# Optimization experiments

Hardware: AMD Instinct MI355X
Metric: run time of the kernel (lower is better)

Reference implementation:

```python
import math
import jax, jax.numpy as jnp
import numpy as np

N, T, D, H = 256, 128, 1024, 1024


def setup_inputs() -> dict:
    key = jax.random.key(0)
    k1, k2, k3, k4, k5 = jax.random.split(key, 5)
    x = jax.random.normal(k1, (N, T, D), dtype=jnp.float32)
    A = jax.random.normal(k2, (N, H, 4, 4), dtype=jnp.float32)
    Wx = jax.random.normal(k3, (D, 4 * H), dtype=jnp.float32) / math.sqrt(D)
    Wh = jax.random.normal(k4, (H, 4 * H), dtype=jnp.float32) / math.sqrt(H)
    Wattn = jax.random.normal(k5, (H, 4 * H), dtype=jnp.float32) / math.sqrt(H)
    b = jnp.zeros((4 * H,), dtype=jnp.float32)
    return {"x": x, "A": A, "Wx": Wx, "Wh": Wh, "Wattn": Wattn, "b": b}


def reference(x, A, Wx, Wh, Wattn, b):
    n, h = A.shape[0], A.shape[1]
    Af = A.reshape(n, h, 16)           # (N, H, 16) flattened 4x4 feature map
    h0 = Af.mean(axis=2)               # mean-pooled global feature inits h0, c0
    scale = 1.0 / math.sqrt(h)

    def step(carry, x_t):
        prev_h, prev_c = carry
        # scaled dot-product attention over 16 spatial locations
        logits = jnp.einsum("nh,nhl->nl", prev_h, Af) * scale   # (N, 16)
        w = jax.nn.softmax(logits, axis=1)
        attn = jnp.einsum("nhl,nl->nh", Af, w)                  # (N, H)
        # LSTM gates
        pre = x_t @ Wx + prev_h @ Wh + attn @ Wattn + b          # (N, 4H)
        i, f, o, g = jnp.split(pre, 4, axis=1)
        next_c = jax.nn.sigmoid(f) * prev_c + jax.nn.sigmoid(i) * jnp.tanh(g)
        next_h = jax.nn.sigmoid(o) * jnp.tanh(next_c)
        return (next_h, next_c), next_h

    xs = jnp.swapaxes(x, 0, 1)         # (T, N, D)
    _, hs = jax.lax.scan(step, (h0, h0), xs)
    return jnp.swapaxes(hs, 0, 1)      # (N, T, H)
```

## Files before the change

kernel.cpp:

```cpp
#include <hip/hip_runtime.h>
#include <hip/hip_bf16.h>

#define NB 256
#define TT 128
#define DD 1024
#define HH 1024
#define FH 4096
#define KTOT 3072

typedef __attribute__((ext_vector_type(4))) float f32x4;
typedef __attribute__((ext_vector_type(8))) short short8;
typedef __attribute__((ext_vector_type(4))) unsigned u32x4;

__device__ __forceinline__ unsigned short f2bf(float f) {
    union { float f; unsigned u; } v; v.f = f;
    unsigned u = v.u;
    u += 0x7FFFu + ((u >> 16) & 1u);
    return (unsigned short)(u >> 16);
}
__device__ __forceinline__ float bf2f(unsigned short u) {
    union { unsigned u; float f; } v; v.u = ((unsigned)u) << 16; return v.f;
}
__device__ __forceinline__ float sigm(float v) { return 1.f / (1.f + __expf(-v)); }
__device__ __forceinline__ float tanhf_(float v) { return 1.f - 2.f / (__expf(2.f * v) + 1.f); }

__device__ __forceinline__ void bmap(int bid, int& m0, int& j0) {
    int xx = bid & 7, yy = (bid >> 3) & 7, mt = bid >> 6;
    m0 = mt * 64;
    j0 = (xx * 8 + yy) * 16;
}

__device__ __forceinline__ short8 pack8(float4 v0, float4 v1) {
    short8 r;
    r[0] = (short)f2bf(v0.x); r[1] = (short)f2bf(v0.y);
    r[2] = (short)f2bf(v0.z); r[3] = (short)f2bf(v0.w);
    r[4] = (short)f2bf(v1.x); r[5] = (short)f2bf(v1.y);
    r[6] = (short)f2bf(v1.z); r[7] = (short)f2bf(v1.w);
    return r;
}

__global__ __launch_bounds__(256) void wt_prep(const float* __restrict__ Wx,
                                               const float* __restrict__ Wh,
                                               const float* __restrict__ Wattn,
                                               unsigned short* __restrict__ Wt) {
    __shared__ unsigned short tile[64][65];
    int k0 = blockIdx.x * 64;
    int c0 = blockIdx.y * 64;
    const float* src; int kl0;
    if (k0 < 1024)      { src = Wx;    kl0 = k0; }
    else if (k0 < 2048) { src = Wh;    kl0 = k0 - 1024; }
    else                { src = Wattn; kl0 = k0 - 2048; }
    int tid = threadIdx.x;
    int r = tid >> 2;
    int ch = (tid & 3) << 4;
    const float* p = src + (size_t)(kl0 + r) * FH + c0 + ch;
#pragma unroll
    for (int i = 0; i < 16; i += 4) {
        float4 v = *reinterpret_cast<const float4*>(p + i);
        tile[r][ch + i + 0] = f2bf(v.x);
        tile[r][ch + i + 1] = f2bf(v.y);
        tile[r][ch + i + 2] = f2bf(v.z);
        tile[r][ch + i + 3] = f2bf(v.w);
    }
    __syncthreads();
    alignas(16) unsigned short vals[16];
#pragma unroll
    for (int i = 0; i < 16; ++i) vals[i] = tile[ch + i][r];
    unsigned short* q = Wt + (size_t)(c0 + r) * KTOT + k0 + ch;
    *reinterpret_cast<uint4*>(q)     = *reinterpret_cast<uint4*>(&vals[0]);
    *reinterpret_cast<uint4*>(q + 8) = *reinterpret_cast<uint4*>(&vals[8]);
}

__global__ __launch_bounds__(256) void zero_buf(float* __restrict__ p, int n) {
    int i = blockIdx.x * 256 + threadIdx.x;
    if (i < n) p[i] = 0.f;
}

__global__ __launch_bounds__(256) void xconv(const float* __restrict__ x,
                                             unsigned short* __restrict__ xbf) {
    size_t i = ((size_t)blockIdx.x * 256 + threadIdx.x) * 8;
    float4 v0 = *reinterpret_cast<const float4*>(x + i);
    float4 v1 = *reinterpret_cast<const float4*>(x + i + 4);
    short8 p = pack8(v0, v1);
    *reinterpret_cast<short8*>(xbf + i) = p;
}

__global__ __launch_bounds__(256) void afT_prep(const float* __restrict__ A,
                                                unsigned short* __restrict__ AfT) {
    int n = blockIdx.x;
#pragma unroll
    for (int pass = 0; pass < 4; ++pass) {
        int hh = pass * 256 + threadIdx.x;
        const float4* p = reinterpret_cast<const float4*>(A + ((size_t)n * HH + hh) * 16);
        float4 a0 = p[0], a1 = p[1], a2 = p[2], a3 = p[3];
        float av[16] = {a0.x,a0.y,a0.z,a0.w, a1.x,a1.y,a1.z,a1.w,
                        a2.x,a2.y,a2.z,a2.w, a3.x,a3.y,a3.z,a3.w};
#pragma unroll
        for (int l = 0; l < 16; ++l)
            AfT[((size_t)n * 16 + l) * HH + hh] = f2bf(av[l]);
    }
}

__global__ __launch_bounds__(256) void g_gemm(const unsigned short* __restrict__ AfT,
                                              const unsigned short* __restrict__ Wt,
                                              unsigned short* __restrict__ G) {
    int mt = blockIdx.y;
    int ct = blockIdx.x;
    int tid = threadIdx.x;
    int w = tid >> 6, lane = tid & 63;
    int wm = w >> 1, wn = w & 1;
    int cw = lane & 15, k8 = (lane >> 4) << 3;

    const unsigned short* ap[4];
    const unsigned short* bp[4];
#pragma unroll
    for (int mf = 0; mf < 4; ++mf)
        ap[mf] = AfT + (size_t)(mt * 128 + wm * 64 + mf * 16 + cw) * HH + k8;
#pragma unroll
    for (int fn = 0; fn < 4; ++fn)
        bp[fn] = Wt + (size_t)(ct * 128 + wn * 64 + fn * 16 + cw) * KTOT + 2048 + k8;

    f32x4 acc[4][4];
#pragma unroll
    for (int mf = 0; mf < 4; ++mf)
#pragma unroll
        for (int fn = 0; fn < 4; ++fn)
#pragma unroll
            for (int e = 0; e < 4; ++e) acc[mf][fn][e] = 0.f;

#pragma unroll 4
    for (int ch = 0; ch < 32; ++ch) {
        short8 a[4], b[4];
#pragma unroll
        for (int i = 0; i < 4; ++i)
            a[i] = *reinterpret_cast<const short8*>(ap[i] + ch * 32);
#pragma unroll
        for (int i = 0; i < 4; ++i)
            b[i] = *reinterpret_cast<const short8*>(bp[i] + ch * 32);
#pragma unroll
        for (int mf = 0; mf < 4; ++mf)
#pragma unroll
            for (int fn = 0; fn < 4; ++fn)
                acc[mf][fn] = __builtin_amdgcn_mfma_f32_16x16x32_bf16(
                    a[mf], b[fn], acc[mf][fn], 0, 0, 0);
    }

    int l0 = (lane >> 4) << 2;
#pragma unroll
    for (int mf = 0; mf < 4; ++mf) {
        int n = mt * 8 + wm * 4 + mf;
#pragma unroll
        for (int fn = 0; fn < 4; ++fn) {
            int cc = ct * 128 + wn * 64 + fn * 16 + cw;
            unsigned lo = (unsigned)f2bf(acc[mf][fn][0]) | ((unsigned)f2bf(acc[mf][fn][1]) << 16);
            unsigned hi = (unsigned)f2bf(acc[mf][fn][2]) | ((unsigned)f2bf(acc[mf][fn][3]) << 16);
            uint2 val; val.x = lo; val.y = hi;
            *reinterpret_cast<uint2*>(G + ((size_t)n * FH + cc) * 16 + l0) = val;
        }
    }
}

template<bool PF32>
__global__ __launch_bounds__(256)
void xw_gemm(const float* __restrict__ x, const unsigned short* __restrict__ Wt,
             const float* __restrict__ bb, void* __restrict__ prex) {
    int ct = blockIdx.x;
    int mt = blockIdx.y;
    int tid = threadIdx.x;
    int w = tid >> 6, lane = tid & 63;
    int wm = w >> 1, wn = w & 1;
    int cw = lane & 15, k8 = (lane >> 4) << 3;

    const float* ap[4];
    const unsigned short* bp[4];
#pragma unroll
    for (int mf = 0; mf < 4; ++mf)
        ap[mf] = x + (size_t)(mt * 128 + wm * 64 + mf * 16 + cw) * DD + k8;
#pragma unroll
    for (int fn = 0; fn < 4; ++fn)
        bp[fn] = Wt + (size_t)(ct * 128 + wn * 64 + fn * 16 + cw) * KTOT + k8;

    f32x4 acc[4][4];
#pragma unroll
    for (int mf = 0; mf < 4; ++mf)
#pragma unroll
        for (int fn = 0; fn < 4; ++fn)
#pragma unroll
            for (int e = 0; e < 4; ++e) acc[mf][fn][e] = 0.f;

#pragma unroll 2
    for (int ch = 0; ch < 32; ++ch) {
        short8 a[4]; short8 b[4];
#pragma unroll
        for (int i = 0; i < 4; ++i) {
            float4 u0 = *reinterpret_cast<const float4*>(ap[i] + ch * 32);
            float4 u1 = *reinterpret_cast<const float4*>(ap[i] + ch * 32 + 4);
            a[i] = pack8(u0, u1);
        }
#pragma unroll
        for (int i = 0; i < 4; ++i)
            b[i] = *reinterpret_cast<const short8*>(bp[i] + ch * 32);
#pragma unroll
        for (int mf = 0; mf < 4; ++mf)
#pragma unroll
            for (int fn = 0; fn < 4; ++fn)
                acc[mf][fn] = __builtin_amdgcn_mfma_f32_16x16x32_bf16(
                    a[mf], b[fn], acc[mf][fn], 0, 0, 0);
    }

    int r0 = (lane >> 4) << 2;
#pragma unroll
    for (int fn = 0; fn < 4; ++fn) {
        int cc = ct * 128 + wn * 64 + fn * 16 + cw;
        float bv = bb[cc];
#pragma unroll
        for (int mf = 0; mf < 4; ++mf) {
            size_t row = (size_t)(mt * 128 + wm * 64 + mf * 16 + r0);
#pragma unroll
            for (int e = 0; e < 4; ++e) {
                float v = acc[mf][fn][e] + bv;
                if (PF32) ((float*)prex)[(row + e) * FH + cc] = v;
                else      ((unsigned short*)prex)[(row + e) * FH + cc] = f2bf(v);
            }
        }
    }
}

__global__ __launch_bounds__(512) void init_kernel(const float* __restrict__ A,
                                                   float* __restrict__ c,
                                                   unsigned short* __restrict__ h0,
                                                   float* __restrict__ lg0) {
    int m0, j0; bmap(blockIdx.x, m0, j0);
    int tid = threadIdx.x;
    int r = tid >> 3, j2 = (tid & 7) * 2;
    int n = m0 + r;
    float lg[16];
#pragma unroll
    for (int l = 0; l < 16; ++l) lg[l] = 0.f;
#pragma unroll
    for (int e = 0; e < 2; ++e) {
        int j = j0 + j2 + e;
        const float4* p = reinterpret_cast<const float4*>(A + ((size_t)n * HH + j) * 16);
        float4 a0 = p[0], a1 = p[1], a2 = p[2], a3 = p[3];
        float av[16] = {a0.x,a0.y,a0.z,a0.w, a1.x,a1.y,a1.z,a1.w,
                        a2.x,a2.y,a2.z,a2.w, a3.x,a3.y,a3.z,a3.w};
        float s = 0.f;
#pragma unroll
        for (int l = 0; l < 16; ++l) s += av[l];
        float m = s * 0.0625f;
        c[(size_t)n * HH + j] = m;
        h0[(size_t)n * HH + j] = f2bf(m);
#pragma unroll
        for (int l = 0; l < 16; ++l) lg[l] += m * av[l];
    }
#pragma unroll
    for (int l = 0; l < 16; ++l) {
        lg[l] += __shfl_xor(lg[l], 1);
        lg[l] += __shfl_xor(lg[l], 2);
        lg[l] += __shfl_xor(lg[l], 4);
    }
    int l0 = (tid & 7) * 2;
    atomicAdd(&lg0[(size_t)n * 16 + l0],     lg[l0]);
    atomicAdd(&lg0[(size_t)n * 16 + l0 + 1], lg[l0 + 1]);
}

template<bool PF32>
__global__ __launch_bounds__(256, 4)
void step_prex(const void* __restrict__ prex,
               const unsigned short* __restrict__ hprev, unsigned short* __restrict__ hnext,
               const unsigned short* __restrict__ Wt, const unsigned short* __restrict__ G,
               const unsigned short* __restrict__ AfT,
               const float* __restrict__ lgcur, float* __restrict__ lgnext,
               float* __restrict__ lgz, float* __restrict__ c,
               float* __restrict__ out, int t) {
    __shared__ float red[2][64][20];
    __shared__ float hn_s[16][16];

    const int bid = blockIdx.x;
    const int jt = (bid & 7) * 8 + ((bid >> 3) & 7);
    const int mt = bid >> 6;
    const int m0 = mt * 16, j0 = jt * 16;
    const int tid = threadIdx.x;
    const int wk = tid >> 6, lane = tid & 63;
    const int cw = lane & 15, k8 = (lane >> 4) << 3;

    const unsigned short* bp[4];
#pragma unroll
    for (int fn = 0; fn < 4; ++fn)
        bp[fn] = Wt + (size_t)(fn * 1024 + j0 + cw) * KTOT + 1024 + wk * 256 + k8;
    const unsigned short* ap = hprev + (size_t)(m0 + cw) * HH + wk * 256 + k8;

    f32x4 acc[4];
#pragma unroll
    for (int fn = 0; fn < 4; ++fn)
#pragma unroll
        for (int e = 0; e < 4; ++e) acc[fn][e] = 0.f;

#pragma unroll
    for (int ch = 0; ch < 8; ++ch) {
        short8 a = *reinterpret_cast<const short8*>(ap + ch * 32);
        short8 b[4];
#pragma unroll
        for (int i = 0; i < 4; ++i)
            b[i] = *reinterpret_cast<const short8*>(bp[i] + ch * 32);
#pragma unroll
        for (int fn = 0; fn < 4; ++fn)
            acc[fn] = __builtin_amdgcn_mfma_f32_16x16x32_bf16(a, b[fn], acc[fn], 0, 0, 0);
    }

    const int r0 = (lane >> 4) << 2;
    if (wk < 2) {
#pragma unroll
        for (int fn = 0; fn < 4; ++fn)
            *reinterpret_cast<f32x4*>(&red[wk][fn * 16 + cw][r0]) = acc[fn];
    }
    __syncthreads();
    if (wk >= 2) {
#pragma unroll
        for (int fn = 0; fn < 4; ++fn) {
            float* p = &red[wk - 2][fn * 16 + cw][r0];
            f32x4 v = *reinterpret_cast<const f32x4*>(p);
            v += acc[fn];
            *reinterpret_cast<f32x4*>(p) = v;
        }
    }
    __syncthreads();

    const int er = tid >> 4, ej = tid & 15;
    const int en = m0 + er, ejj = j0 + ej;

    const u32x4* gb = reinterpret_cast<const u32x4*>(G + ((size_t)en * FH + ejj) * 16);
    u32x4 gv[8];
#pragma unroll
    for (int g = 0; g < 4; ++g) {
        gv[g * 2]     = gb[g * 2048];
        gv[g * 2 + 1] = gb[g * 2048 + 1];
    }
    float pxv[4];
    {
        size_t prow = ((size_t)en * TT + t) * FH + ejj;
#pragma unroll
        for (int g = 0; g < 4; ++g) {
            if (PF32) pxv[g] = ((const float*)prex)[prow + g * 1024];
            else      pxv[g] = bf2f(((const unsigned short*)prex)[prow + g * 1024]);
        }
    }
    float cv = c[(size_t)en * HH + ejj];

    float sm[16];
    {
        const float4* lp = reinterpret_cast<const float4*>(lgcur + (size_t)en * 16);
        float4 s0 = lp[0], s1 = lp[1], s2 = lp[2], s3 = lp[3];
        float sv[16] = {s0.x,s0.y,s0.z,s0.w, s1.x,s1.y,s1.z,s1.w,
                        s2.x,s2.y,s2.z,s2.w, s3.x,s3.y,s3.z,s3.w};
        float mx = -1e30f;
#pragma unroll
        for (int l = 0; l < 16; ++l) { sv[l] *= 0.03125f; mx = fmaxf(mx, sv[l]); }
        float sum = 0.f;
#pragma unroll
        for (int l = 0; l < 16; ++l) { sm[l] = __expf(sv[l] - mx); sum += sm[l]; }
        float inv = 1.f / sum;
#pragma unroll
        for (int l = 0; l < 16; ++l) sm[l] *= inv;
    }

    float pre[4];
#pragma unroll
    for (int g = 0; g < 4; ++g) {
        float p = red[0][g * 16 + ej][er] + red[1][g * 16 + ej][er] + pxv[g];
        float d = 0.f;
#pragma unroll
        for (int q = 0; q < 4; ++q) {
            d += sm[q * 2]     * bf2f((unsigned short)(gv[g * 2][q] & 0xFFFF));
            d += sm[q * 2 + 1] * bf2f((unsigned short)(gv[g * 2][q] >> 16));
        }
#pragma unroll
        for (int q = 0; q < 4; ++q) {
            d += sm[8 + q * 2]     * bf2f((unsigned short)(gv[g * 2 + 1][q] & 0xFFFF));
            d += sm[8 + q * 2 + 1] * bf2f((unsigned short)(gv[g * 2 + 1][q] >> 16));
        }
        pre[g] = p + d;
    }

    float ig = sigm(pre[0]);
    float fg = sigm(pre[1]);
    float og = sigm(pre[2]);
    float gg = tanhf_(pre[3]);
    float cn = fg * cv + ig * gg;
    float hn = og * tanhf_(cn);
    c[(size_t)en * HH + ejj] = cn;
    hnext[(size_t)en * HH + ejj] = f2bf(hn);
    __builtin_nontemporal_store(hn, out + ((size_t)en * TT + t) * HH + ejj);
    hn_s[er][ej] = hn;
    if (jt == 0) lgz[(size_t)en * 16 + ej] = 0.f;
    __syncthreads();

    const unsigned short* afp = AfT + ((size_t)en * 16 + ej) * HH + j0;
    uint4 q0 = *reinterpret_cast<const uint4*>(afp);
    uint4 q1 = *reinterpret_cast<const uint4*>(afp + 8);
    const unsigned* au = reinterpret_cast<const unsigned*>(&q0);
    const unsigned* av = reinterpret_cast<const unsigned*>(&q1);
    float part = 0.f;
#pragma unroll
    for (int q = 0; q < 4; ++q) {
        part += hn_s[er][q * 2]     * bf2f((unsigned short)(au[q] & 0xFFFF));
        part += hn_s[er][q * 2 + 1] * bf2f((unsigned short)(au[q] >> 16));
    }
#pragma unroll
    for (int q = 0; q < 4; ++q) {
        part += hn_s[er][8 + q * 2]     * bf2f((unsigned short)(av[q] & 0xFFFF));
        part += hn_s[er][8 + q * 2 + 1] * bf2f((unsigned short)(av[q] >> 16));
    }
    atomicAdd(&lgnext[(size_t)en * 16 + ej], part);
}

template<bool XBF>
__global__ __launch_bounds__(256, 4)
void gemm_step(const float* __restrict__ x, const unsigned short* __restrict__ xbf,
               const unsigned short* __restrict__ hprev, unsigned short* __restrict__ hnext,
               const unsigned short* __restrict__ Wt, const unsigned short* __restrict__ G,
               const unsigned short* __restrict__ AfT, const float* __restrict__ bb,
               const float* __restrict__ lgcur, float* __restrict__ lgnext,
               float* __restrict__ lgz, float* __restrict__ c,
               float* __restrict__ out, int t) {
    __shared__ float red[2][64][36];
    __shared__ float hn_s[32][16];

    const int bid = blockIdx.x;
    const int jt = (bid & 7) * 8 + ((bid >> 3) & 7);
    const int mt = bid >> 6;
    const int m0 = mt * 32, j0 = jt * 16;
    const int tid = threadIdx.x;
    const int wk = tid >> 6, lane = tid & 63;
    const int cw = lane & 15, k8 = (lane >> 4) << 3;

    const unsigned short* bp[4];
#pragma unroll
    for (int fn = 0; fn < 4; ++fn)
        bp[fn] = Wt + (size_t)(fn * 1024 + j0 + cw) * KTOT + wk * 512 + k8;

    f32x4 acc[2][4];
#pragma unroll
    for (int mf = 0; mf < 2; ++mf)
#pragma unroll
        for (int fn = 0; fn < 4; ++fn)
#pragma unroll
            for (int e = 0; e < 4; ++e) acc[mf][fn][e] = 0.f;

    if (wk < 2) {
        if (XBF) {
            const unsigned short* ap[2];
#pragma unroll
            for (int mf = 0; mf < 2; ++mf)
                ap[mf] = xbf + ((size_t)(m0 + mf * 16 + cw) * TT + t) * DD + wk * 512 + k8;
#pragma unroll 4
            for (int ch = 0; ch < 16; ++ch) {
                short8 a[2], b[4];
#pragma unroll
                for (int i = 0; i < 2; ++i)
                    a[i] = *reinterpret_cast<const short8*>(ap[i] + ch * 32);
#pragma unroll
                for (int i = 0; i < 4; ++i)
                    b[i] = *reinterpret_cast<const short8*>(bp[i] + ch * 32);
#pragma unroll
                for (int mf = 0; mf < 2; ++mf)
#pragma unroll
                    for (int fn = 0; fn < 4; ++fn)
                        acc[mf][fn] = __builtin_amdgcn_mfma_f32_16x16x32_bf16(
                            a[mf], b[fn], acc[mf][fn], 0, 0, 0);
            }
        } else {
            const float* ap[2];
#pragma unroll
            for (int mf = 0; mf < 2; ++mf)
                ap[mf] = x + ((size_t)(m0 + mf * 16 + cw) * TT + t) * DD + wk * 512 + k8;
#pragma unroll 2
            for (int ch = 0; ch < 16; ++ch) {
                short8 a[2], b[4];
#pragma unroll
                for (int i = 0; i < 2; ++i) {
                    float4 u0 = *reinterpret_cast<const float4*>(ap[i] + ch * 32);
                    float4 u1 = *reinterpret_cast<const float4*>(ap[i] + ch * 32 + 4);
                    a[i] = pack8(u0, u1);
                }
#pragma unroll
                for (int i = 0; i < 4; ++i)
                    b[i] = *reinterpret_cast<const short8*>(bp[i] + ch * 32);
#pragma unroll
                for (int mf = 0; mf < 2; ++mf)
#pragma unroll
                    for (int fn = 0; fn < 4; ++fn)
                        acc[mf][fn] = __builtin_amdgcn_mfma_f32_16x16x32_bf16(
                            a[mf], b[fn], acc[mf][fn], 0, 0, 0);
            }
        }
    } else {
        const unsigned short* ap[2];
#pragma unroll
        for (int mf = 0; mf < 2; ++mf)
            ap[mf] = hprev + (size_t)(m0 + mf * 16 + cw) * HH + (wk - 2) * 512 + k8;
#pragma unroll 4
        for (int ch = 0; ch < 16; ++ch) {
            short8 a[2], b[4];
#pragma unroll
            for (int i = 0; i < 2; ++i)
                a[i] = *reinterpret_cast<const short8*>(ap[i] + ch * 32);
#pragma unroll
            for (int i = 0; i < 4; ++i)
                b[i] = *reinterpret_cast<const short8*>(bp[i] + ch * 32);
#pragma unroll
            for (int mf = 0; mf < 2; ++mf)
#pragma unroll
                for (int fn = 0; fn < 4; ++fn)
                    acc[mf][fn] = __builtin_amdgcn_mfma_f32_16x16x32_bf16(
                        a[mf], b[fn], acc[mf][fn], 0, 0, 0);
        }
    }

    const int r0 = (lane >> 4) << 2;
    if (wk < 2) {
#pragma unroll
        for (int mf = 0; mf < 2; ++mf)
#pragma unroll
            for (int fn = 0; fn < 4; ++fn)
                *reinterpret_cast<f32x4*>(&red[wk][fn * 16 + cw][mf * 16 + r0]) = acc[mf][fn];
    }
    __syncthreads();
    if (wk >= 2) {
#pragma unroll
        for (int mf = 0; mf < 2; ++mf)
#pragma unroll
            for (int fn = 0; fn < 4; ++fn) {
                float* p = &red[wk - 2][fn * 16 + cw][mf * 16 + r0];
                f32x4 v = *reinterpret_cast<const f32x4*>(p);
                v += acc[mf][fn];
                *reinterpret_cast<f32x4*>(p) = v;
            }
    }
    __syncthreads();

    const bool zeroer = (jt == 0);
#pragma unroll
    for (int s = 0; s < 2; ++s) {
        int task = tid + s * 256;
        int er = task >> 4, ej = task & 15;
        int en = m0 + er, ejj = j0 + ej;

        const u32x4* gb = reinterpret_cast<const u32x4*>(G + ((size_t)en * FH + ejj) * 16);
        u32x4 gv[8];
#pragma unroll
        for (int g = 0; g < 4; ++g) {
            gv[g * 2]     = gb[g * 2048];
            gv[g * 2 + 1] = gb[g * 2048 + 1];
        }
        float cv = c[(size_t)en * HH + ejj];

        float sm[16];
        {
            const float4* lp = reinterpret_cast<const float4*>(lgcur + (size_t)en * 16);
            float4 s0 = lp[0], s1 = lp[1], s2 = lp[2], s3 = lp[3];
            float sv[16] = {s0.x,s0.y,s0.z,s0.w, s1.x,s1.y,s1.z,s1.w,
                            s2.x,s2.y,s2.z,s2.w, s3.x,s3.y,s3.z,s3.w};
            float mx = -1e30f;
#pragma unroll
            for (int l = 0; l < 16; ++l) { sv[l] *= 0.03125f; mx = fmaxf(mx, sv[l]); }
            float sum = 0.f;
#pragma unroll
            for (int l = 0; l < 16; ++l) { sm[l] = __expf(sv[l] - mx); sum += sm[l]; }
            float inv = 1.f / sum;
#pragma unroll
            for (int l = 0; l < 16; ++l) sm[l] *= inv;
        }

        float pre[4];
#pragma unroll
        for (int g = 0; g < 4; ++g) {
            float p = red[0][g * 16 + ej][er] + red[1][g * 16 + ej][er] + bb[g * HH + ejj];
            float d = 0.f;
#pragma unroll
            for (int q = 0; q < 4; ++q) {
                d += sm[q * 2]     * bf2f((unsigned short)(gv[g * 2][q] & 0xFFFF));
                d += sm[q * 2 + 1] * bf2f((unsigned short)(gv[g * 2][q] >> 16));
            }
#pragma unroll
            for (int q = 0; q < 4; ++q) {
                d += sm[8 + q * 2]     * bf2f((unsigned short)(gv[g * 2 + 1][q] & 0xFFFF));
                d += sm[8 + q * 2 + 1] * bf2f((unsigned short)(gv[g * 2 + 1][q] >> 16));
            }
            pre[g] = p + d;
        }

        float ig = sigm(pre[0]);
        float fg = sigm(pre[1]);
        float og = sigm(pre[2]);
        float gg = tanhf_(pre[3]);
        float cn = fg * cv + ig * gg;
        float hn = og * tanhf_(cn);
        c[(size_t)en * HH + ejj] = cn;
        hnext[(size_t)en * HH + ejj] = f2bf(hn);
        __builtin_nontemporal_store(hn, out + ((size_t)en * TT + t) * HH + ejj);
        hn_s[er][ej] = hn;
        if (zeroer) lgz[(size_t)en * 16 + ej] = 0.f;
    }
    __syncthreads();

#pragma unroll
    for (int s = 0; s < 2; ++s) {
        int task = tid + s * 256;
        int er = task >> 4, ej = task & 15;
        int en = m0 + er;
        const unsigned short* afp = AfT + ((size_t)en * 16 + ej) * HH + j0;
        uint4 q0 = *reinterpret_cast<const uint4*>(afp);
        uint4 q1 = *reinterpret_cast<const uint4*>(afp + 8);
        const unsigned* au = reinterpret_cast<const unsigned*>(&q0);
        const unsigned* av = reinterpret_cast<const unsigned*>(&q1);
        float part = 0.f;
#pragma unroll
        for (int q = 0; q < 4; ++q) {
            part += hn_s[er][q * 2]     * bf2f((unsigned short)(au[q] & 0xFFFF));
            part += hn_s[er][q * 2 + 1] * bf2f((unsigned short)(au[q] >> 16));
        }
#pragma unroll
        for (int q = 0; q < 4; ++q) {
            part += hn_s[er][8 + q * 2]     * bf2f((unsigned short)(av[q] & 0xFFFF));
            part += hn_s[er][8 + q * 2 + 1] * bf2f((unsigned short)(av[q] >> 16));
        }
        atomicAdd(&lgnext[(size_t)en * 16 + ej], part);
    }
}

extern "C" void kernel_launch(void* const* d_in, const int* in_sizes, int n_in,
                              void* d_out, int out_size, void* d_ws, size_t ws_size,
                              hipStream_t stream) {
    const float* x     = (const float*)d_in[0];
    const float* A     = (const float*)d_in[1];
    const float* Wx    = (const float*)d_in[2];
    const float* Wh    = (const float*)d_in[3];
    const float* Wattn = (const float*)d_in[4];
    const float* bptr  = (const float*)d_in[5];
    float* out = (float*)d_out;

    char* ws = (char*)d_ws;
    unsigned short* Wt   = (unsigned short*)(ws);
    unsigned short* G    = (unsigned short*)(ws + 25165824);
    unsigned short* AfT  = (unsigned short*)(ws + 58720256);
    unsigned short* hbuf = (unsigned short*)(ws + 67108864);
    float* c             = (float*)(ws + 68157440);
    float* lg            = (float*)(ws + 69206016);
    const size_t base = 69255168;
    void* prex = (void*)(ws + base);
    unsigned short* xbf = (unsigned short*)(ws + base);

    bool prex32 = ws_size >= base + (size_t)536870912;
    bool prex16 = !prex32 && ws_size >= base + (size_t)268435456;
    bool use_xbf = !prex32 && !prex16 && ws_size >= base + (size_t)67108864;

    wt_prep<<<dim3(48, 64), 256, 0, stream>>>(Wx, Wh, Wattn, Wt);
    zero_buf<<<48, 256, 0, stream>>>(lg, 3 * NB * 16);
    afT_prep<<<NB, 256, 0, stream>>>(A, AfT);
    g_gemm<<<dim3(32, 32), 256, 0, stream>>>(AfT, Wt, G);
    init_kernel<<<256, 512, 0, stream>>>(A, c, hbuf, lg);
    if (prex32)      xw_gemm<true><<<dim3(32, 256), 256, 0, stream>>>(x, Wt, bptr, prex);
    else if (prex16) xw_gemm<false><<<dim3(32, 256), 256, 0, stream>>>(x, Wt, bptr, prex);
    else if (use_xbf) xconv<<<16384, 256, 0, stream>>>(x, xbf);

    for (int t = 0; t < TT; ++t) {
        const unsigned short* hp = hbuf + (size_t)(t & 1) * NB * HH;
        unsigned short* hx       = hbuf + (size_t)((t & 1) ^ 1) * NB * HH;
        const float* lgc = lg + (size_t)(t % 3) * NB * 16;
        float* lgn       = lg + (size_t)((t + 1) % 3) * NB * 16;
        float* lgzz      = lg + (size_t)((t + 2) % 3) * NB * 16;
        if (prex32)
            step_prex<true><<<1024, 256, 0, stream>>>(prex, hp, hx, Wt, G, AfT,
                                                      lgc, lgn, lgzz, c, out, t);
        else if (prex16)
            step_prex<false><<<1024, 256, 0, stream>>>(prex, hp, hx, Wt, G, AfT,
                                                       lgc, lgn, lgzz, c, out, t);
        else if (use_xbf)
            gemm_step<true><<<512, 256, 0, stream>>>(x, xbf, hp, hx, Wt, G, AfT, bptr,
                                                     lgc, lgn, lgzz, c, out, t);
        else
            gemm_step<false><<<512, 256, 0, stream>>>(x, xbf, hp, hx, Wt, G, AfT, bptr,
                                                      lgc, lgn, lgzz, c, out, t);
    }
}
```

Before: 4.818 ms.

## Overlap x@Wx projection with recurrent steps by computing timesteps ahead

```diff
diff --git a/kernel.cpp b/kernel.cpp
--- a/kernel.cpp
+++ b/kernel.cpp
@@ -160,29 +160,27 @@
     }
 }
 
-template<bool PF32>
-__global__ __launch_bounds__(256)
-void xw_gemm(const float* __restrict__ x, const unsigned short* __restrict__ Wt,
-             const float* __restrict__ bb, void* __restrict__ prex) {
-    int ct = blockIdx.x;
-    int mt = blockIdx.y;
-    int tid = threadIdx.x;
+__device__ __forceinline__ void xw_tile(int nb, int ct, int tx, int tid,
+                                        const float* __restrict__ x,
+                                        const unsigned short* __restrict__ Wt,
+                                        const float* __restrict__ bb,
+                                        unsigned short* __restrict__ prex) {
     int w = tid >> 6, lane = tid & 63;
     int wm = w >> 1, wn = w & 1;
     int cw = lane & 15, k8 = (lane >> 4) << 3;
 
-    const float* ap[4];
+    const float* ap[2];
     const unsigned short* bp[4];
 #pragma unroll
-    for (int mf = 0; mf < 4; ++mf)
-        ap[mf] = x + (size_t)(mt * 128 + wm * 64 + mf * 16 + cw) * DD + k8;
+    for (int mf = 0; mf < 2; ++mf)
+        ap[mf] = x + ((size_t)(nb * 64 + wm * 32 + mf * 16 + cw) * TT + tx) * DD + k8;
 #pragma unroll
     for (int fn = 0; fn < 4; ++fn)
         bp[fn] = Wt + (size_t)(ct * 128 + wn * 64 + fn * 16 + cw) * KTOT + k8;
 
-    f32x4 acc[4][4];
-#pragma unroll
-    for (int mf = 0; mf < 4; ++mf)
+    f32x4 acc[2][4];
+#pragma unroll
+    for (int mf = 0; mf < 2; ++mf)
 #pragma unroll
         for (int fn = 0; fn < 4; ++fn)
 #pragma unroll
@@ -190,9 +188,9 @@
 
 #pragma unroll 2
     for (int ch = 0; ch < 32; ++ch) {
-        short8 a[4]; short8 b[4];
-#pragma unroll
-        for (int i = 0; i < 4; ++i) {
+        short8 a[2], b[4];
+#pragma unroll
+        for (int i = 0; i < 2; ++i) {
             float4 u0 = *reinterpret_cast<const float4*>(ap[i] + ch * 32);
             float4 u1 = *reinterpret_cast<const float4*>(ap[i] + ch * 32 + 4);
             a[i] = pack8(u0, u1);
@@ -201,7 +199,7 @@
         for (int i = 0; i < 4; ++i)
             b[i] = *reinterpret_cast<const short8*>(bp[i] + ch * 32);
 #pragma unroll
-        for (int mf = 0; mf < 4; ++mf)
+        for (int mf = 0; mf < 2; ++mf)
 #pragma unroll
             for (int fn = 0; fn < 4; ++fn)
                 acc[mf][fn] = __builtin_amdgcn_mfma_f32_16x16x32_bf16(
@@ -214,16 +212,22 @@
         int cc = ct * 128 + wn * 64 + fn * 16 + cw;
         float bv = bb[cc];
 #pragma unroll
-        for (int mf = 0; mf < 4; ++mf) {
-            size_t row = (size_t)(mt * 128 + wm * 64 + mf * 16 + r0);
+        for (int mf = 0; mf < 2; ++mf) {
+            int nrow = nb * 64 + wm * 32 + mf * 16 + r0;
 #pragma unroll
             for (int e = 0; e < 4; ++e) {
                 float v = acc[mf][fn][e] + bv;
-                if (PF32) ((float*)prex)[(row + e) * FH + cc] = v;
-                else      ((unsigned short*)prex)[(row + e) * FH + cc] = f2bf(v);
+                __builtin_nontemporal_store(
+                    f2bf(v), prex + ((size_t)(nrow + e) * TT + tx) * FH + cc);
             }
         }
     }
+}
+
+__global__ __launch_bounds__(256)
+void xw_pro(const float* __restrict__ x, const unsigned short* __restrict__ Wt,
+            const float* __restrict__ bb, unsigned short* __restrict__ prex) {
+    xw_tile(blockIdx.x >> 5, blockIdx.x & 31, blockIdx.y, threadIdx.x, x, Wt, bb, prex);
 }
 
 __global__ __launch_bounds__(512) void init_kernel(const float* __restrict__ A,
@@ -264,12 +268,13 @@
     atomicAdd(&lg0[(size_t)n * 16 + l0 + 1], lg[l0 + 1]);
 }
 
-template<bool PF32>
 __global__ __launch_bounds__(256, 4)
-void step_prex(const void* __restrict__ prex,
+void step_prex(const float* __restrict__ x,
+               const unsigned short* __restrict__ prexc,
+               unsigned short* __restrict__ prex,
                const unsigned short* __restrict__ hprev, unsigned short* __restrict__ hnext,
                const unsigned short* __restrict__ Wt, const unsigned short* __restrict__ G,
-               const unsigned short* __restrict__ AfT,
+               const unsigned short* __restrict__ AfT, const float* __restrict__ bb,
                const float* __restrict__ lgcur, float* __restrict__ lgnext,
                float* __restrict__ lgz, float* __restrict__ c,
                float* __restrict__ out, int t) {
@@ -277,10 +282,18 @@
     __shared__ float hn_s[16][16];
 
     const int bid = blockIdx.x;
+    const int tid = threadIdx.x;
+
+    if (bid >= 1024) {
+        int xb = bid - 1024;
+        int tx = t + 4;
+        if (tx < TT) xw_tile(xb >> 5, xb & 31, tx, tid, x, Wt, bb, prex);
+        return;
+    }
+
     const int jt = (bid & 7) * 8 + ((bid >> 3) & 7);
     const int mt = bid >> 6;
     const int m0 = mt * 16, j0 = jt * 16;
-    const int tid = threadIdx.x;
     const int wk = tid >> 6, lane = tid & 63;
     const int cw = lane & 15, k8 = (lane >> 4) << 3;
 
@@ -340,10 +353,8 @@
     {
         size_t prow = ((size_t)en * TT + t) * FH + ejj;
 #pragma unroll
-        for (int g = 0; g < 4; ++g) {
-            if (PF32) pxv[g] = ((const float*)prex)[prow + g * 1024];
-            else      pxv[g] = bf2f(((const unsigned short*)prex)[prow + g * 1024]);
-        }
+        for (int g = 0; g < 4; ++g)
+            pxv[g] = bf2f(__builtin_nontemporal_load(prexc + prow + g * 1024));
     }
     float cv = c[(size_t)en * HH + ejj];
 
@@ -648,20 +659,18 @@
     float* c             = (float*)(ws + 68157440);
     float* lg            = (float*)(ws + 69206016);
     const size_t base = 69255168;
-    void* prex = (void*)(ws + base);
-    unsigned short* xbf = (unsigned short*)(ws + base);
-
-    bool prex32 = ws_size >= base + (size_t)536870912;
-    bool prex16 = !prex32 && ws_size >= base + (size_t)268435456;
-    bool use_xbf = !prex32 && !prex16 && ws_size >= base + (size_t)67108864;
+    unsigned short* prex = (unsigned short*)(ws + base);
+    unsigned short* xbf  = (unsigned short*)(ws + base);
+
+    bool prex16  = ws_size >= base + (size_t)268435456;
+    bool use_xbf = !prex16 && ws_size >= base + (size_t)67108864;
 
     wt_prep<<<dim3(48, 64), 256, 0, stream>>>(Wx, Wh, Wattn, Wt);
     zero_buf<<<48, 256, 0, stream>>>(lg, 3 * NB * 16);
     afT_prep<<<NB, 256, 0, stream>>>(A, AfT);
     g_gemm<<<dim3(32, 32), 256, 0, stream>>>(AfT, Wt, G);
     init_kernel<<<256, 512, 0, stream>>>(A, c, hbuf, lg);
-    if (prex32)      xw_gemm<true><<<dim3(32, 256), 256, 0, stream>>>(x, Wt, bptr, prex);
-    else if (prex16) xw_gemm<false><<<dim3(32, 256), 256, 0, stream>>>(x, Wt, bptr, prex);
+    if (prex16)       xw_pro<<<dim3(128, 4), 256, 0, stream>>>(x, Wt, bptr, prex);
     else if (use_xbf) xconv<<<16384, 256, 0, stream>>>(x, xbf);
 
     for (int t = 0; t < TT; ++t) {
@@ -670,12 +679,9 @@
         const float* lgc = lg + (size_t)(t % 3) * NB * 16;
         float* lgn       = lg + (size_t)((t + 1) % 3) * NB * 16;
         float* lgzz      = lg + (size_t)((t + 2) % 3) * NB * 16;
-        if (prex32)
-            step_prex<true><<<1024, 256, 0, stream>>>(prex, hp, hx, Wt, G, AfT,
-                                                      lgc, lgn, lgzz, c, out, t);
-        else if (prex16)
-            step_prex<false><<<1024, 256, 0, stream>>>(prex, hp, hx, Wt, G, AfT,
-                                                       lgc, lgn, lgzz, c, out, t);
+        if (prex16)
+            step_prex<<<1152, 256, 0, stream>>>(x, prex, prex, hp, hx, Wt, G, AfT, bptr,
+                                                lgc, lgn, lgzz, c, out, t);
         else if (use_xbf)
             gemm_step<true><<<512, 256, 0, stream>>>(x, xbf, hp, hx, Wt, G, AfT, bptr,
                                                      lgc, lgn, lgzz, c, out, t);
```

Result: slower. 7.526 ms (+56.2%).
